# Kernel tuning notes

Measured on AMD Instinct MI355X. Metric: run time of the kernel, lower is better.

## Reference

```python
import jax, jax.numpy as jnp
import numpy as np

B, M, C, S, SD, K, H = 32, 448, 384, 512, 128, 8, 8
DH = C // H
EPS = 1e-5
NEG_SLOPE = 0.2


def setup_inputs() -> dict:
    key = jax.random.key(0)
    ks = iter(jax.random.split(key, 32))
    nrm = lambda shape, scale=0.05: (jax.random.normal(next(ks), shape, jnp.float32) * scale)
    inp = {
        'q': jax.random.normal(next(ks), (B, M, C), jnp.float32),
        'coarse': jax.random.normal(next(ks), (B, M, 3), jnp.float32),
        'skeleton': jax.random.normal(next(ks), (B, S, 3), jnp.float32),
        # GraphConv 1: 3 -> 64 (root weight, rel/neighbor weight, bias)
        'gc1_wroot': nrm((3, 64), 0.3), 'gc1_wrel': nrm((3, 64), 0.3), 'gc1_b': jnp.zeros((64,), jnp.float32),
        # GraphConv 2: 64 -> SD
        'gc2_wroot': nrm((64, SD), 0.1), 'gc2_wrel': nrm((64, SD), 0.1), 'gc2_b': jnp.zeros((SD,), jnp.float32),
        # skeleton_projection: SD -> C
        'proj_w': nrm((SD, C), 0.08), 'proj_b': jnp.zeros((C,), jnp.float32),
        # MultiheadAttention (torch layout: in_proj (3C, C), out_proj (C, C))
        'attn_in_w': nrm((3 * C, C), 0.05), 'attn_in_b': jnp.zeros((3 * C,), jnp.float32),
        'attn_out_w': nrm((C, C), 0.05), 'attn_out_b': jnp.zeros((C,), jnp.float32),
        # increase_dim: Conv1d(C,1024,1) + BN(1024) + LeakyReLU + Conv1d(1024,1024,1)
        'inc1_w': nrm((1024, C), 0.05), 'inc1_b': jnp.zeros((1024,), jnp.float32),
        'bn_g': jnp.ones((1024,), jnp.float32), 'bn_b': jnp.zeros((1024,), jnp.float32),
        'bn_m': jnp.zeros((1024,), jnp.float32), 'bn_v': jnp.ones((1024,), jnp.float32),
        'inc2_w': nrm((1024, 1024), 0.03), 'inc2_b': jnp.zeros((1024,), jnp.float32),
        # reduce_map: Linear(C + 1024 + 3, C)
        'red_w': nrm((1024 + C + 3, C), 0.03), 'red_b': jnp.zeros((C,), jnp.float32),
    }
    return inp


def _knn_idx(pts):
    # pts: [B,S,3]; per-batch kNN (self excluded), matching knn_graph(k=K, batch=...)
    d2 = jnp.sum((pts[:, :, None, :] - pts[:, None, :, :]) ** 2, axis=-1)  # [B,S,S]
    d2 = d2 + jnp.eye(S, dtype=pts.dtype)[None] * 1e10                       # mask self
    _, idx = jax.lax.top_k(-d2, K)                                           # [B,S,K]
    return idx


def _graph_conv(x, idx, wroot, wrel, b):
    # GraphConv (PyG, aggr='add'): out_i = x_i Wroot + (sum_{j in N(i)} x_j) Wrel + b
    nb = jax.vmap(lambda f, i: f[i])(x, idx)   # [B,S,K,F]
    agg = nb.sum(axis=2)                       # [B,S,F]
    return x @ wroot + agg @ wrel + b


def reference(q, coarse, skeleton, gc1_wroot, gc1_wrel, gc1_b, gc2_wroot, gc2_wrel, gc2_b,
              proj_w, proj_b, attn_in_w, attn_in_b, attn_out_w, attn_out_b,
              inc1_w, inc1_b, bn_g, bn_b, bn_m, bn_v, inc2_w, inc2_b, red_w, red_b):
    # --- skeleton branch: knn graph + 2-layer GraphConv + max-pool + projection ---
    idx = _knn_idx(skeleton)
    h = _graph_conv(skeleton, idx, gc1_wroot, gc1_wrel, gc1_b)
    h = jax.nn.relu(h)
    h = _graph_conv(h, idx, gc2_wroot, gc2_wrel, gc2_b)        # [B,S,SD]
    proxy = jnp.max(h, axis=1)                                  # [B,SD]
    proxy = proxy @ proj_w + proj_b                             # [B,C]
    kv = jnp.broadcast_to(proxy[:, None, :], (B, M, C))         # expanded proxies

    # --- cross attention (torch nn.MultiheadAttention math) ---
    wq, wk, wv = attn_in_w[:C], attn_in_w[C:2 * C], attn_in_w[2 * C:]
    bq, bk, bv = attn_in_b[:C], attn_in_b[C:2 * C], attn_in_b[2 * C:]
    qh = (q @ wq.T + bq).reshape(B, M, H, DH)
    kh = (kv @ wk.T + bk).reshape(B, M, H, DH)
    vh = (kv @ wv.T + bv).reshape(B, M, H, DH)
    scores = jnp.einsum('bmhd,bnhd->bhmn', qh, kh) / jnp.sqrt(jnp.float32(DH))
    attn = jax.nn.softmax(scores, axis=-1)
    ctx = jnp.einsum('bhmn,bnhd->bmhd', attn, vh).reshape(B, M, C)
    q = ctx @ attn_out_w.T + attn_out_b                         # fused features [B,M,C]

    # --- increase_dim (1x1 conv == matmul) + BN(eval) + LeakyReLU + 1x1 conv ---
    g = jnp.einsum('bmc,oc->bmo', q, inc1_w) + inc1_b           # [B,M,1024]
    g = bn_g * (g - bn_m) * jax.lax.rsqrt(bn_v + EPS) + bn_b
    g = jnp.where(g >= 0, g, NEG_SLOPE * g)
    g = jnp.einsum('bmc,oc->bmo', g, inc2_w) + inc2_b
    global_feature = jnp.max(g, axis=1)                         # [B,1024]

    # --- concat + reduce_map ---
    rebuild = jnp.concatenate([jnp.broadcast_to(global_feature[:, None, :], (B, M, 1024)), q, coarse], axis=-1)
    out = rebuild @ red_w + red_b                               # [B,M,C]
    return out
```

## Files before the change

kernel.cpp:

```cpp
#include <hip/hip_runtime.h>

#define NB 32
#define MM 448
#define CC 384
#define SS 512
#define KNN 8

#define WS_IDX   0u
#define WS_H1    524288u
#define WS_PMAX  (WS_H1 + 4194304u)
#define WS_Q     (WS_PMAX + 262144u)
#define WS_Y     (WS_Q + 49152u)
#define WS_G2    (WS_Y + 131072u)
#define WS_BASEP (WS_G2 + 131072u)
#define WS_KV    WS_IDX
#define WS_VV    (WS_IDX + 49152u)
#define WS_PP    WS_H1

__device__ __forceinline__ float wave_sum(float v) {
#pragma unroll
  for (int m = 1; m < 64; m <<= 1) v += __shfl_xor(v, m, 64);
  return v;
}

__global__ __launch_bounds__(256) void k_knn_gc1(
    const float* __restrict__ skel,
    const float* __restrict__ w1root, const float* __restrict__ w1rel,
    const float* __restrict__ b1,
    int* __restrict__ idx_ws, float* __restrict__ h1_ws)
{
  int b   = blockIdx.x >> 7;
  int grp = blockIdx.x & 127;
  __shared__ __align__(16) float4 sk[SS];
  const float* sb = skel + b * SS * 3;
  for (int t = threadIdx.x; t < SS; t += 256)
    sk[t] = make_float4(sb[t*3+0], sb[t*3+1], sb[t*3+2], 0.f);
  __syncthreads();

  int wave = threadIdx.x >> 6, lane = threadIdx.x & 63;
  int i = grp * 4 + wave;
  float4 pi = sk[i];

  float bd[KNN];
#pragma unroll
  for (int t = 0; t < KNN; t++) {
    int j = lane + (t << 6);
    float4 p = sk[j];
    float d2;
    {
#pragma clang fp contract(off)
      float dx = pi.x - p.x, dy = pi.y - p.y, dz = pi.z - p.z;
      d2 = (dx*dx + dy*dy) + dz*dz;
    }
    bd[t] = (j == i) ? 3e38f : d2;
  }

  int win[KNN];
  int* idx_base = idx_ws + (size_t)(b*SS + i) * KNN;
#pragma unroll
  for (int t = 0; t < KNN; t++) {
    float bestd = bd[0]; int bests = 0;
#pragma unroll
    for (int s = 1; s < KNN; s++)
      if (bd[s] < bestd) { bestd = bd[s]; bests = s; }
    int bestj = lane + (bests << 6);
#pragma unroll
    for (int m = 1; m < 64; m <<= 1) {
      float od = __shfl_xor(bestd, m, 64);
      int   oj = __shfl_xor(bestj, m, 64);
      if (od < bestd || (od == bestd && oj < bestj)) { bestd = od; bestj = oj; }
    }
    win[t] = bestj;
    if (lane == t) idx_base[t] = bestj;
    if ((bestj & 63) == lane) {
      int sl = bestj >> 6;
#pragma unroll
      for (int s = 0; s < KNN; s++) if (s == sl) bd[s] = 3e38f;
    }
  }

  float a0 = 0.f, a1 = 0.f, a2 = 0.f;
#pragma unroll
  for (int t = 0; t < KNN; t++) {
    float4 n = sk[win[t]];
    a0 += n.x; a1 += n.y; a2 += n.z;
  }

  int c = lane;
  float h = b1[c] + pi.x*w1root[c] + pi.y*w1root[64+c] + pi.z*w1root[128+c]
                  + a0*w1rel[c]   + a1*w1rel[64+c]   + a2*w1rel[128+c];
  h = fmaxf(h, 0.f);
  h1_ws[(size_t)(b*SS + i) * 64 + lane] = h;
}

__global__ __launch_bounds__(256) void k_gc2_max(
    const float* __restrict__ h1_ws, const int* __restrict__ idx_ws,
    const float* __restrict__ w2root, const float* __restrict__ w2rel,
    const float* __restrict__ b2, float* __restrict__ pmax)
{
  int b = blockIdx.x, chunk = blockIdx.y;
  int i0 = chunk * 64;
  __shared__ __align__(16) float smem[12992];
  float* wroot_s = smem;
  float* wrel_s  = smem + 4128;
  float* hr_s    = smem + 8256;
  float* ag_s    = smem + 10368;
  int*   nbs     = (int*)(smem + 12480);

  const float* h1b = h1_ws + (size_t)b * SS * 64;

  nbs[threadIdx.x]       = idx_ws[(b*SS + i0)*KNN + threadIdx.x];
  nbs[threadIdx.x + 256] = idx_ws[(b*SS + i0)*KNN + threadIdx.x + 256];

  int rg = threadIdx.x >> 3, og = threadIdx.x & 7;
  int r0 = rg*2, r1 = rg*2 + 1;
  float acc0[16], acc1[16];
#pragma unroll
  for (int u = 0; u < 16; u++) { acc0[u] = 0.f; acc1[u] = 0.f; }

  for (int p = 0; p < 2; p++) {
    __syncthreads();
#pragma unroll
    for (int p2 = 0; p2 < 16; p2++) {
      int idx = threadIdx.x + 256*p2;
      int kk = idx >> 7, c = idx & 127;
      int ogs = c >> 4, j = c & 15;
      int dst = ogs*516 + kk*16 + j;
      int srco = (p*32 + kk)*128 + c;
      wroot_s[dst] = w2root[srco];
      wrel_s[dst]  = w2rel[srco];
    }
#pragma unroll
    for (int p2 = 0; p2 < 8; p2++) {
      int idx = threadIdx.x + 256*p2;
      int r = idx >> 5, kk = idx & 31;
      hr_s[r*33 + kk] = h1b[(i0 + r)*64 + p*32 + kk];
      float s = 0.f;
#pragma unroll
      for (int k = 0; k < KNN; k++)
        s += h1b[nbs[r*8 + k]*64 + p*32 + kk];
      ag_s[r*33 + kk] = s;
    }
    __syncthreads();
    const float* wr = wroot_s + og*516;
    const float* wl = wrel_s  + og*516;
#pragma unroll 2
    for (int kk = 0; kk < 32; kk++) {
      float h0 = hr_s[r0*33 + kk], h1v = hr_s[r1*33 + kk];
      float a0 = ag_s[r0*33 + kk], a1v = ag_s[r1*33 + kk];
      float4 R0 = *(const float4*)(wr + kk*16);
      float4 R1 = *(const float4*)(wr + kk*16 + 4);
      float4 R2 = *(const float4*)(wr + kk*16 + 8);
      float4 R3 = *(const float4*)(wr + kk*16 + 12);
      float4 L0 = *(const float4*)(wl + kk*16);
      float4 L1 = *(const float4*)(wl + kk*16 + 4);
      float4 L2 = *(const float4*)(wl + kk*16 + 8);
      float4 L3 = *(const float4*)(wl + kk*16 + 12);
      acc0[0]+=h0*R0.x+a0*L0.x;  acc1[0]+=h1v*R0.x+a1v*L0.x;
      acc0[1]+=h0*R0.y+a0*L0.y;  acc1[1]+=h1v*R0.y+a1v*L0.y;
      acc0[2]+=h0*R0.z+a0*L0.z;  acc1[2]+=h1v*R0.z+a1v*L0.z;
      acc0[3]+=h0*R0.w+a0*L0.w;  acc1[3]+=h1v*R0.w+a1v*L0.w;
      acc0[4]+=h0*R1.x+a0*L1.x;  acc1[4]+=h1v*R1.x+a1v*L1.x;
      acc0[5]+=h0*R1.y+a0*L1.y;  acc1[5]+=h1v*R1.y+a1v*L1.y;
      acc0[6]+=h0*R1.z+a0*L1.z;  acc1[6]+=h1v*R1.z+a1v*L1.z;
      acc0[7]+=h0*R1.w+a0*L1.w;  acc1[7]+=h1v*R1.w+a1v*L1.w;
      acc0[8]+=h0*R2.x+a0*L2.x;  acc1[8]+=h1v*R2.x+a1v*L2.x;
      acc0[9]+=h0*R2.y+a0*L2.y;  acc1[9]+=h1v*R2.y+a1v*L2.y;
      acc0[10]+=h0*R2.z+a0*L2.z; acc1[10]+=h1v*R2.z+a1v*L2.z;
      acc0[11]+=h0*R2.w+a0*L2.w; acc1[11]+=h1v*R2.w+a1v*L2.w;
      acc0[12]+=h0*R3.x+a0*L3.x; acc1[12]+=h1v*R3.x+a1v*L3.x;
      acc0[13]+=h0*R3.y+a0*L3.y; acc1[13]+=h1v*R3.y+a1v*L3.y;
      acc0[14]+=h0*R3.z+a0*L3.z; acc1[14]+=h1v*R3.z+a1v*L3.z;
      acc0[15]+=h0*R3.w+a0*L3.w; acc1[15]+=h1v*R3.w+a1v*L3.w;
    }
  }
  __syncthreads();
  float* m = smem;
#pragma unroll
  for (int u = 0; u < 16; u++)
    m[rg*128 + og*16 + u] = fmaxf(acc0[u], acc1[u]);
  __syncthreads();
  if (threadIdx.x < 128) {
    int col = threadIdx.x;
    float mx = -3e38f;
#pragma unroll 8
    for (int g = 0; g < 32; g++) mx = fmaxf(mx, m[g*128 + col]);
    pmax[(b*8 + chunk)*128 + col] = mx + b2[col];
  }
}

__global__ __launch_bounds__(384) void k_proxy_kv(
    const float* __restrict__ pmax,
    const float* __restrict__ proj_w, const float* __restrict__ proj_b,
    float* __restrict__ kv_ws)
{
  int b = blockIdx.x, t = threadIdx.x;
  __shared__ float proxy[128];
  if (t < 128) {
    float m = -3e38f;
    for (int ch = 0; ch < 8; ch++) m = fmaxf(m, pmax[(b*8 + ch)*128 + t]);
    proxy[t] = m;
  }
  __syncthreads();
  float acc = proj_b[t];
  for (int s = 0; s < 128; s++) acc += proxy[s] * proj_w[s*CC + t];
  kv_ws[b*CC + t] = acc;
}

__global__ __launch_bounds__(256) void k_mv384(
    const float* __restrict__ xin, const float* __restrict__ w, int row0,
    const float* __restrict__ bias, int bias0, float* __restrict__ out)
{
  int b = blockIdx.x, og = blockIdx.y;
  int wv = threadIdx.x >> 6, lane = threadIdx.x & 63;
  __shared__ float xs[CC];
  for (int t = threadIdx.x; t < CC; t += 256) xs[t] = xin[b*CC + t];
  __syncthreads();
  float x0 = xs[lane*6+0], x1 = xs[lane*6+1], x2 = xs[lane*6+2];
  float x3 = xs[lane*6+3], x4 = xs[lane*6+4], x5 = xs[lane*6+5];
#pragma unroll
  for (int u = 0; u < 8; u++) {
    int o = og*32 + wv*8 + u;
    const float* wr = w + (size_t)(row0 + o) * CC + lane*6;
    float2 wa = *(const float2*)wr;
    float2 wb = *(const float2*)(wr + 2);
    float2 wc = *(const float2*)(wr + 4);
    float p = wa.x*x0 + wa.y*x1 + wb.x*x2 + wb.y*x3 + wc.x*x4 + wc.y*x5;
    p = wave_sum(p);
    if (lane == 0) out[b*CC + o] = bias[bias0 + o] + p;
  }
}

__global__ __launch_bounds__(256) void k_inc1_bn(
    const float* __restrict__ q_ws, const float* __restrict__ inc1_w,
    const float* __restrict__ inc1_b,
    const float* __restrict__ bng, const float* __restrict__ bnb,
    const float* __restrict__ bnm, const float* __restrict__ bnv,
    float* __restrict__ y_ws)
{
  int b = blockIdx.x >> 5, og = blockIdx.x & 31;
  int wv = threadIdx.x >> 6, lane = threadIdx.x & 63;
  __shared__ float xs[CC];
  for (int t = threadIdx.x; t < CC; t += 256) xs[t] = q_ws[b*CC + t];
  __syncthreads();
  float x0 = xs[lane*6+0], x1 = xs[lane*6+1], x2 = xs[lane*6+2];
  float x3 = xs[lane*6+3], x4 = xs[lane*6+4], x5 = xs[lane*6+5];
#pragma unroll
  for (int u = 0; u < 8; u++) {
    int o = og*32 + wv*8 + u;
    const float* wr = inc1_w + (size_t)o * CC + lane*6;
    float2 wa = *(const float2*)wr;
    float2 wb = *(const float2*)(wr + 2);
    float2 wc = *(const float2*)(wr + 4);
    float p = wa.x*x0 + wa.y*x1 + wb.x*x2 + wb.y*x3 + wc.x*x4 + wc.y*x5;
    p = wave_sum(p);
    if (lane == 0) {
      float acc = p + inc1_b[o];
      float z = bng[o] * (acc - bnm[o]) * rsqrtf(bnv[o] + 1e-5f) + bnb[o];
      y_ws[b*1024 + o] = (z >= 0.f) ? z : 0.2f * z;
    }
  }
}

__global__ __launch_bounds__(256) void k_inc2(
    const float* __restrict__ y_ws, const float* __restrict__ inc2_w,
    const float* __restrict__ inc2_b, float* __restrict__ g2_ws)
{
  int b = blockIdx.x >> 5, og = blockIdx.x & 31;
  int wv = threadIdx.x >> 6, lane = threadIdx.x & 63;
  __shared__ __align__(16) float xs[1024];
  for (int t = threadIdx.x; t < 1024; t += 256) xs[t] = y_ws[b*1024 + t];
  __syncthreads();
  float4 X0 = *(const float4*)(xs + lane*16 + 0);
  float4 X1 = *(const float4*)(xs + lane*16 + 4);
  float4 X2 = *(const float4*)(xs + lane*16 + 8);
  float4 X3 = *(const float4*)(xs + lane*16 + 12);
#pragma unroll
  for (int u = 0; u < 8; u++) {
    int o = og*32 + wv*8 + u;
    const float* wr = inc2_w + (size_t)o * 1024 + lane*16;
    float4 W0 = *(const float4*)(wr + 0);
    float4 W1 = *(const float4*)(wr + 4);
    float4 W2 = *(const float4*)(wr + 8);
    float4 W3 = *(const float4*)(wr + 12);
    float p = W0.x*X0.x + W0.y*X0.y + W0.z*X0.z + W0.w*X0.w
            + W1.x*X1.x + W1.y*X1.y + W1.z*X1.z + W1.w*X1.w
            + W2.x*X2.x + W2.y*X2.y + W2.z*X2.z + W2.w*X2.w
            + W3.x*X3.x + W3.y*X3.y + W3.z*X3.z + W3.w*X3.w;
    p = wave_sum(p);
    if (lane == 0) g2_ws[b*1024 + o] = p + inc2_b[o];
  }
}

__global__ __launch_bounds__(256) void k_basep(
    const float* __restrict__ g2_ws, const float* __restrict__ q_ws,
    const float* __restrict__ red_w, float* __restrict__ pp)
{
  int cg = blockIdx.x;
  int o0 = blockIdx.y * 64;
  int c0 = cg * 32;
  __shared__ __align__(16) float xs[32*33];
  __shared__ __align__(16) float wt[32*64];
#pragma unroll
  for (int p = 0; p < 8; p++) {
    int idx = threadIdx.x + 256*p;
    int c = idx >> 6, o = idx & 63;
    wt[idx] = red_w[(size_t)(c0 + c)*CC + o0 + o];
  }
  {
    int b = threadIdx.x >> 3, cp = threadIdx.x & 7;
    const float* src = (cg < 32) ? (g2_ws + b*1024 + c0)
                                 : (q_ws  + b*CC   + (c0 - 1024));
    float4 v = *(const float4*)(src + cp*4);
    xs[(cp*4+0)*33 + b] = v.x;
    xs[(cp*4+1)*33 + b] = v.y;
    xs[(cp*4+2)*33 + b] = v.z;
    xs[(cp*4+3)*33 + b] = v.w;
  }
  __syncthreads();
  int b = threadIdx.x >> 3, og = threadIdx.x & 7;
  float acc[8];
#pragma unroll
  for (int u = 0; u < 8; u++) acc[u] = 0.f;
#pragma unroll 8
  for (int c = 0; c < 32; c++) {
    float xv = xs[c*33 + b];
    float4 w0 = *(const float4*)(wt + c*64 + og*8);
    float4 w1 = *(const float4*)(wt + c*64 + og*8 + 4);
    acc[0] += xv*w0.x; acc[1] += xv*w0.y; acc[2] += xv*w0.z; acc[3] += xv*w0.w;
    acc[4] += xv*w1.x; acc[5] += xv*w1.y; acc[6] += xv*w1.z; acc[7] += xv*w1.w;
  }
  float* dst = pp + (size_t)(cg*32 + b)*CC + o0 + og*8;
  *(float4*)dst       = make_float4(acc[0], acc[1], acc[2], acc[3]);
  *(float4*)(dst + 4) = make_float4(acc[4], acc[5], acc[6], acc[7]);
}

__global__ __launch_bounds__(256) void k_base_red(
    const float* __restrict__ pp, float* __restrict__ basep)
{
  int idx = blockIdx.x * 256 + threadIdx.x;
  float s = 0.f;
#pragma unroll 4
  for (int cg = 0; cg < 44; cg++) s += pp[cg*12288 + idx];
  basep[idx] = s;
}

__global__ __launch_bounds__(256) void k_out(
    const float* __restrict__ basep, const float* __restrict__ red_b,
    const float* __restrict__ red_w, const float* __restrict__ coarse,
    float* __restrict__ out)
{
  int gid = blockIdx.x * 256 + threadIdx.x;
  int c4 = gid % 96;
  int row = gid / 96;
  int b = row / 448;
  int c = c4 * 4;
  float4 p0 = *(const float4*)(basep + b*CC + c);
  float4 rb = *(const float4*)(red_b + c);
  const float* cr = coarse + (size_t)row * 3;
  float cx = cr[0], cy = cr[1], cz = cr[2];
  float4 w0 = *(const float4*)(red_w + (size_t)1408*CC + c);
  float4 w1 = *(const float4*)(red_w + (size_t)1409*CC + c);
  float4 w2 = *(const float4*)(red_w + (size_t)1410*CC + c);
  float4 o4;
  o4.x = p0.x + rb.x + cx*w0.x + cy*w1.x + cz*w2.x;
  o4.y = p0.y + rb.y + cx*w0.y + cy*w1.y + cz*w2.y;
  o4.z = p0.z + rb.z + cx*w0.z + cy*w1.z + cz*w2.z;
  o4.w = p0.w + rb.w + cx*w0.w + cy*w1.w + cz*w2.w;
  *(float4*)(out + (size_t)row*CC + c) = o4;
}

extern "C" void kernel_launch(void* const* d_in, const int* in_sizes, int n_in,
                              void* d_out, int out_size, void* d_ws, size_t ws_size,
                              hipStream_t stream)
{
  (void)in_sizes; (void)n_in; (void)out_size; (void)ws_size;
  const float* coarse = (const float*)d_in[1];
  const float* skel   = (const float*)d_in[2];
  const float* g1wr   = (const float*)d_in[3];
  const float* g1wl   = (const float*)d_in[4];
  const float* g1b    = (const float*)d_in[5];
  const float* g2wr   = (const float*)d_in[6];
  const float* g2wl   = (const float*)d_in[7];
  const float* g2b    = (const float*)d_in[8];
  const float* projw  = (const float*)d_in[9];
  const float* projb  = (const float*)d_in[10];
  const float* aiw    = (const float*)d_in[11];
  const float* aib    = (const float*)d_in[12];
  const float* aow    = (const float*)d_in[13];
  const float* aob    = (const float*)d_in[14];
  const float* i1w    = (const float*)d_in[15];
  const float* i1b    = (const float*)d_in[16];
  const float* bng    = (const float*)d_in[17];
  const float* bnb    = (const float*)d_in[18];
  const float* bnm    = (const float*)d_in[19];
  const float* bnv    = (const float*)d_in[20];
  const float* i2w    = (const float*)d_in[21];
  const float* i2b    = (const float*)d_in[22];
  const float* redw   = (const float*)d_in[23];
  const float* redb   = (const float*)d_in[24];
  float* out = (float*)d_out;

  char* ws = (char*)d_ws;
  int*   idx_ws = (int*)(ws + WS_IDX);
  float* h1_ws  = (float*)(ws + WS_H1);
  float* pmax   = (float*)(ws + WS_PMAX);
  float* q_ws   = (float*)(ws + WS_Q);
  float* y_ws   = (float*)(ws + WS_Y);
  float* g2_ws  = (float*)(ws + WS_G2);
  float* basep  = (float*)(ws + WS_BASEP);
  float* kv_ws  = (float*)(ws + WS_KV);
  float* vv_ws  = (float*)(ws + WS_VV);
  float* pp     = (float*)(ws + WS_PP);

  k_knn_gc1<<<4096, 256, 0, stream>>>(skel, g1wr, g1wl, g1b, idx_ws, h1_ws);
  k_gc2_max<<<dim3(32, 8), 256, 0, stream>>>(h1_ws, idx_ws, g2wr, g2wl, g2b, pmax);
  k_proxy_kv<<<32, 384, 0, stream>>>(pmax, projw, projb, kv_ws);
  k_mv384<<<dim3(32, 12), 256, 0, stream>>>(kv_ws, aiw, 2*CC, aib, 2*CC, vv_ws);
  k_mv384<<<dim3(32, 12), 256, 0, stream>>>(vv_ws, aow, 0,    aob, 0,    q_ws);
  k_inc1_bn<<<1024, 256, 0, stream>>>(q_ws, i1w, i1b, bng, bnb, bnm, bnv, y_ws);
  k_inc2<<<1024, 256, 0, stream>>>(y_ws, i2w, i2b, g2_ws);
  k_basep<<<dim3(44, 6), 256, 0, stream>>>(g2_ws, q_ws, redw, pp);
  k_base_red<<<48, 256, 0, stream>>>(pp, basep);
  k_out<<<5376, 256, 0, stream>>>(basep, redb, redw, coarse, out);
}
```

Baseline: 256.6 us.

## Retile graph-conv2 max over more blocks and fuse attention mat-vec chain

k_gc2_max is reorganized to use 32-row chunks (512 blocks instead of 256), with root and neighbor-sum features concatenated into one 128-wide K operand in shared memory and a 4x4 register tile per thread. The proxy projection and the two attention mat-vecs (value projection, output projection) are merged into a single per-batch kernel, removing two launches and the global round trips for the intermediate vectors. The trade-off is that the fused chain runs on only 32 blocks, so each block reads the full 384x384 weight matrices twice, which may be slower than the earlier 384-block mat-vec launches.

```diff
diff --git a/kernel.cpp b/kernel.cpp
--- a/kernel.cpp
+++ b/kernel.cpp
@@ -13,8 +13,6 @@
 #define WS_Y     (WS_Q + 49152u)
 #define WS_G2    (WS_Y + 131072u)
 #define WS_BASEP (WS_G2 + 131072u)
-#define WS_KV    WS_IDX
-#define WS_VV    (WS_IDX + 49152u)
 #define WS_PP    WS_H1
 
 __device__ __forceinline__ float wave_sum(float v) {
@@ -98,136 +96,134 @@
     const float* __restrict__ w2root, const float* __restrict__ w2rel,
     const float* __restrict__ b2, float* __restrict__ pmax)
 {
-  int b = blockIdx.x, chunk = blockIdx.y;
-  int i0 = chunk * 64;
-  __shared__ __align__(16) float smem[12992];
-  float* wroot_s = smem;
-  float* wrel_s  = smem + 4128;
-  float* hr_s    = smem + 8256;
-  float* ag_s    = smem + 10368;
-  int*   nbs     = (int*)(smem + 12480);
+  int b = blockIdx.x >> 4, chunk = blockIdx.x & 15;
+  int r0 = chunk * 32;
+  __shared__ __align__(16) float X[32*129];
+  __shared__ __align__(16) float Wt[32*128];
+  __shared__ float mred[8*128];
+  __shared__ int nbs[32*KNN];
 
   const float* h1b = h1_ws + (size_t)b * SS * 64;
-
-  nbs[threadIdx.x]       = idx_ws[(b*SS + i0)*KNN + threadIdx.x];
-  nbs[threadIdx.x + 256] = idx_ws[(b*SS + i0)*KNN + threadIdx.x + 256];
-
-  int rg = threadIdx.x >> 3, og = threadIdx.x & 7;
-  int r0 = rg*2, r1 = rg*2 + 1;
-  float acc0[16], acc1[16];
-#pragma unroll
-  for (int u = 0; u < 16; u++) { acc0[u] = 0.f; acc1[u] = 0.f; }
-
-  for (int p = 0; p < 2; p++) {
+  nbs[threadIdx.x] = idx_ws[(b*SS + r0)*KNN + threadIdx.x];
+#pragma unroll
+  for (int p = 0; p < 8; p++) {
+    int idx = threadIdx.x + 256*p;
+    int r = idx >> 6, k = idx & 63;
+    X[r*129 + k] = h1b[(r0 + r)*64 + k];
+  }
+  __syncthreads();
+#pragma unroll
+  for (int p = 0; p < 8; p++) {
+    int idx = threadIdx.x + 256*p;
+    int r = idx >> 6, k = idx & 63;
+    const int* nb = nbs + r*KNN;
+    float s = 0.f;
+#pragma unroll
+    for (int j = 0; j < KNN; j++) s += h1b[nb[j]*64 + k];
+    X[r*129 + 64 + k] = s;
+  }
+
+  int rg = threadIdx.x >> 5, cg = threadIdx.x & 31;
+  float acc[4][4];
+#pragma unroll
+  for (int r = 0; r < 4; r++)
+#pragma unroll
+    for (int u = 0; u < 4; u++) acc[r][u] = 0.f;
+
+  const float* wsrc[4] = { w2root, w2root + 32*128, w2rel, w2rel + 32*128 };
+#pragma unroll 1
+  for (int ch = 0; ch < 4; ch++) {
     __syncthreads();
-#pragma unroll
-    for (int p2 = 0; p2 < 16; p2++) {
-      int idx = threadIdx.x + 256*p2;
-      int kk = idx >> 7, c = idx & 127;
-      int ogs = c >> 4, j = c & 15;
-      int dst = ogs*516 + kk*16 + j;
-      int srco = (p*32 + kk)*128 + c;
-      wroot_s[dst] = w2root[srco];
-      wrel_s[dst]  = w2rel[srco];
-    }
-#pragma unroll
-    for (int p2 = 0; p2 < 8; p2++) {
-      int idx = threadIdx.x + 256*p2;
-      int r = idx >> 5, kk = idx & 31;
-      hr_s[r*33 + kk] = h1b[(i0 + r)*64 + p*32 + kk];
-      float s = 0.f;
-#pragma unroll
-      for (int k = 0; k < KNN; k++)
-        s += h1b[nbs[r*8 + k]*64 + p*32 + kk];
-      ag_s[r*33 + kk] = s;
+    const float* ws = wsrc[ch];
+#pragma unroll
+    for (int p = 0; p < 16; p++) {
+      int idx = threadIdx.x + 256*p;
+      Wt[idx] = ws[idx];
     }
     __syncthreads();
-    const float* wr = wroot_s + og*516;
-    const float* wl = wrel_s  + og*516;
-#pragma unroll 2
-    for (int kk = 0; kk < 32; kk++) {
-      float h0 = hr_s[r0*33 + kk], h1v = hr_s[r1*33 + kk];
-      float a0 = ag_s[r0*33 + kk], a1v = ag_s[r1*33 + kk];
-      float4 R0 = *(const float4*)(wr + kk*16);
-      float4 R1 = *(const float4*)(wr + kk*16 + 4);
-      float4 R2 = *(const float4*)(wr + kk*16 + 8);
-      float4 R3 = *(const float4*)(wr + kk*16 + 12);
-      float4 L0 = *(const float4*)(wl + kk*16);
-      float4 L1 = *(const float4*)(wl + kk*16 + 4);
-      float4 L2 = *(const float4*)(wl + kk*16 + 8);
-      float4 L3 = *(const float4*)(wl + kk*16 + 12);
-      acc0[0]+=h0*R0.x+a0*L0.x;  acc1[0]+=h1v*R0.x+a1v*L0.x;
-      acc0[1]+=h0*R0.y+a0*L0.y;  acc1[1]+=h1v*R0.y+a1v*L0.y;
-      acc0[2]+=h0*R0.z+a0*L0.z;  acc1[2]+=h1v*R0.z+a1v*L0.z;
-      acc0[3]+=h0*R0.w+a0*L0.w;  acc1[3]+=h1v*R0.w+a1v*L0.w;
-      acc0[4]+=h0*R1.x+a0*L1.x;  acc1[4]+=h1v*R1.x+a1v*L1.x;
-      acc0[5]+=h0*R1.y+a0*L1.y;  acc1[5]+=h1v*R1.y+a1v*L1.y;
-      acc0[6]+=h0*R1.z+a0*L1.z;  acc1[6]+=h1v*R1.z+a1v*L1.z;
-      acc0[7]+=h0*R1.w+a0*L1.w;  acc1[7]+=h1v*R1.w+a1v*L1.w;
-      acc0[8]+=h0*R2.x+a0*L2.x;  acc1[8]+=h1v*R2.x+a1v*L2.x;
-      acc0[9]+=h0*R2.y+a0*L2.y;  acc1[9]+=h1v*R2.y+a1v*L2.y;
-      acc0[10]+=h0*R2.z+a0*L2.z; acc1[10]+=h1v*R2.z+a1v*L2.z;
-      acc0[11]+=h0*R2.w+a0*L2.w; acc1[11]+=h1v*R2.w+a1v*L2.w;
-      acc0[12]+=h0*R3.x+a0*L3.x; acc1[12]+=h1v*R3.x+a1v*L3.x;
-      acc0[13]+=h0*R3.y+a0*L3.y; acc1[13]+=h1v*R3.y+a1v*L3.y;
-      acc0[14]+=h0*R3.z+a0*L3.z; acc1[14]+=h1v*R3.z+a1v*L3.z;
-      acc0[15]+=h0*R3.w+a0*L3.w; acc1[15]+=h1v*R3.w+a1v*L3.w;
-    }
-  }
-  __syncthreads();
-  float* m = smem;
-#pragma unroll
-  for (int u = 0; u < 16; u++)
-    m[rg*128 + og*16 + u] = fmaxf(acc0[u], acc1[u]);
+    int kb = ch * 32;
+    const float* xr0 = X + (rg*4+0)*129 + kb;
+    const float* xr1 = X + (rg*4+1)*129 + kb;
+    const float* xr2 = X + (rg*4+2)*129 + kb;
+    const float* xr3 = X + (rg*4+3)*129 + kb;
+#pragma unroll 4
+    for (int k = 0; k < 32; k++) {
+      float4 w4 = *(const float4*)(Wt + k*128 + cg*4);
+      float x0 = xr0[k], x1 = xr1[k], x2 = xr2[k], x3 = xr3[k];
+      acc[0][0] += x0*w4.x; acc[0][1] += x0*w4.y; acc[0][2] += x0*w4.z; acc[0][3] += x0*w4.w;
+      acc[1][0] += x1*w4.x; acc[1][1] += x1*w4.y; acc[1][2] += x1*w4.z; acc[1][3] += x1*w4.w;
+      acc[2][0] += x2*w4.x; acc[2][1] += x2*w4.y; acc[2][2] += x2*w4.z; acc[2][3] += x2*w4.w;
+      acc[3][0] += x3*w4.x; acc[3][1] += x3*w4.y; acc[3][2] += x3*w4.z; acc[3][3] += x3*w4.w;
+    }
+  }
+#pragma unroll
+  for (int u = 0; u < 4; u++)
+    mred[rg*128 + cg*4 + u] =
+      fmaxf(fmaxf(acc[0][u], acc[1][u]), fmaxf(acc[2][u], acc[3][u]));
   __syncthreads();
   if (threadIdx.x < 128) {
     int col = threadIdx.x;
-    float mx = -3e38f;
-#pragma unroll 8
-    for (int g = 0; g < 32; g++) mx = fmaxf(mx, m[g*128 + col]);
-    pmax[(b*8 + chunk)*128 + col] = mx + b2[col];
-  }
-}
-
-__global__ __launch_bounds__(384) void k_proxy_kv(
+    float mx = mred[col];
+#pragma unroll
+    for (int g = 1; g < 8; g++) mx = fmaxf(mx, mred[g*128 + col]);
+    pmax[(size_t)(b*16 + chunk)*128 + col] = mx + b2[col];
+  }
+}
+
+__global__ __launch_bounds__(384) void k_attn_chain(
     const float* __restrict__ pmax,
     const float* __restrict__ proj_w, const float* __restrict__ proj_b,
-    float* __restrict__ kv_ws)
+    const float* __restrict__ attn_in_w, const float* __restrict__ attn_in_b,
+    const float* __restrict__ attn_out_w, const float* __restrict__ attn_out_b,
+    float* __restrict__ q_ws)
 {
   int b = blockIdx.x, t = threadIdx.x;
   __shared__ float proxy[128];
+  __shared__ float kv[CC];
+  __shared__ float vv[CC];
   if (t < 128) {
     float m = -3e38f;
-    for (int ch = 0; ch < 8; ch++) m = fmaxf(m, pmax[(b*8 + ch)*128 + t]);
+    for (int ch = 0; ch < 16; ch++) m = fmaxf(m, pmax[(size_t)(b*16 + ch)*128 + t]);
     proxy[t] = m;
   }
   __syncthreads();
-  float acc = proj_b[t];
-  for (int s = 0; s < 128; s++) acc += proxy[s] * proj_w[s*CC + t];
-  kv_ws[b*CC + t] = acc;
-}
-
-__global__ __launch_bounds__(256) void k_mv384(
-    const float* __restrict__ xin, const float* __restrict__ w, int row0,
-    const float* __restrict__ bias, int bias0, float* __restrict__ out)
-{
-  int b = blockIdx.x, og = blockIdx.y;
-  int wv = threadIdx.x >> 6, lane = threadIdx.x & 63;
-  __shared__ float xs[CC];
-  for (int t = threadIdx.x; t < CC; t += 256) xs[t] = xin[b*CC + t];
-  __syncthreads();
-  float x0 = xs[lane*6+0], x1 = xs[lane*6+1], x2 = xs[lane*6+2];
-  float x3 = xs[lane*6+3], x4 = xs[lane*6+4], x5 = xs[lane*6+5];
-#pragma unroll
-  for (int u = 0; u < 8; u++) {
-    int o = og*32 + wv*8 + u;
-    const float* wr = w + (size_t)(row0 + o) * CC + lane*6;
-    float2 wa = *(const float2*)wr;
-    float2 wb = *(const float2*)(wr + 2);
-    float2 wc = *(const float2*)(wr + 4);
-    float p = wa.x*x0 + wa.y*x1 + wb.x*x2 + wb.y*x3 + wc.x*x4 + wc.y*x5;
-    p = wave_sum(p);
-    if (lane == 0) out[b*CC + o] = bias[bias0 + o] + p;
+  {
+    float acc = proj_b[t];
+    for (int s = 0; s < 128; s++) acc += proxy[s] * proj_w[s*CC + t];
+    kv[t] = acc;
+  }
+  __syncthreads();
+  int wv = t >> 6, lane = t & 63;
+  {
+    float x0 = kv[lane*6+0], x1 = kv[lane*6+1], x2 = kv[lane*6+2];
+    float x3 = kv[lane*6+3], x4 = kv[lane*6+4], x5 = kv[lane*6+5];
+#pragma unroll 8
+    for (int u = 0; u < 64; u++) {
+      int o = wv*64 + u;
+      const float* wr = attn_in_w + (size_t)(2*CC + o) * CC + lane*6;
+      float2 wa = *(const float2*)wr;
+      float2 wb = *(const float2*)(wr + 2);
+      float2 wc = *(const float2*)(wr + 4);
+      float p = wa.x*x0 + wa.y*x1 + wb.x*x2 + wb.y*x3 + wc.x*x4 + wc.y*x5;
+      p = wave_sum(p);
+      if (lane == 0) vv[o] = attn_in_b[2*CC + o] + p;
+    }
+  }
+  __syncthreads();
+  {
+    float x0 = vv[lane*6+0], x1 = vv[lane*6+1], x2 = vv[lane*6+2];
+    float x3 = vv[lane*6+3], x4 = vv[lane*6+4], x5 = vv[lane*6+5];
+#pragma unroll 8
+    for (int u = 0; u < 64; u++) {
+      int o = wv*64 + u;
+      const float* wr = attn_out_w + (size_t)o * CC + lane*6;
+      float2 wa = *(const float2*)wr;
+      float2 wb = *(const float2*)(wr + 2);
+      float2 wc = *(const float2*)(wr + 4);
+      float p = wa.x*x0 + wa.y*x1 + wb.x*x2 + wb.y*x3 + wc.x*x4 + wc.y*x5;
+      p = wave_sum(p);
+      if (lane == 0) q_ws[b*CC + o] = attn_out_b[o] + p;
+    }
   }
 }
 
@@ -409,15 +405,11 @@
   float* y_ws   = (float*)(ws + WS_Y);
   float* g2_ws  = (float*)(ws + WS_G2);
   float* basep  = (float*)(ws + WS_BASEP);
-  float* kv_ws  = (float*)(ws + WS_KV);
-  float* vv_ws  = (float*)(ws + WS_VV);
   float* pp     = (float*)(ws + WS_PP);
 
   k_knn_gc1<<<4096, 256, 0, stream>>>(skel, g1wr, g1wl, g1b, idx_ws, h1_ws);
-  k_gc2_max<<<dim3(32, 8), 256, 0, stream>>>(h1_ws, idx_ws, g2wr, g2wl, g2b, pmax);
-  k_proxy_kv<<<32, 384, 0, stream>>>(pmax, projw, projb, kv_ws);
-  k_mv384<<<dim3(32, 12), 256, 0, stream>>>(kv_ws, aiw, 2*CC, aib, 2*CC, vv_ws);
-  k_mv384<<<dim3(32, 12), 256, 0, stream>>>(vv_ws, aow, 0,    aob, 0,    q_ws);
+  k_gc2_max<<<512, 256, 0, stream>>>(h1_ws, idx_ws, g2wr, g2wl, g2b, pmax);
+  k_attn_chain<<<32, 384, 0, stream>>>(pmax, projw, projb, aiw, aib, aow, aob, q_ws);
   k_inc1_bn<<<1024, 256, 0, stream>>>(q_ws, i1w, i1b, bng, bnb, bnm, bnv, y_ws);
   k_inc2<<<1024, 256, 0, stream>>>(y_ws, i2w, i2b, g2_ws);
   k_basep<<<dim3(44, 6), 256, 0, stream>>>(g2_ws, q_ws, redw, pp);
```

Measured after the change: 292.0 us. 1.14x slower.
